# Kernel optimization log

Hardware: AMD Instinct MI355X
Metric: run time of the kernel (lower is better)

Reference implementation:

```python
import jax, jax.numpy as jnp
import numpy as np

EMBED_DIM = 512
NUM_HEADS = 8
HEAD_DIM = EMBED_DIM // NUM_HEADS
SCALE = HEAD_DIM ** -0.5
B, N = 4, 2048


def _linear_params(key, fan_in, fan_out):
    kw, kb = jax.random.split(key)
    bound = 1.0 / np.sqrt(fan_in)
    W = jax.random.uniform(kw, (fan_out, fan_in), minval=-bound, maxval=bound, dtype=jnp.float32)
    b = jax.random.uniform(kb, (fan_out,), minval=-bound, maxval=bound, dtype=jnp.float32)
    return W, b


def setup_inputs() -> dict:
    key = jax.random.key(0)
    ks = jax.random.split(key, 7)
    query = jax.random.normal(ks[0], (B, N, EMBED_DIM), dtype=jnp.float32)
    k_in = jax.random.normal(ks[1], (B, N, EMBED_DIM), dtype=jnp.float32)
    v_in = jax.random.normal(ks[2], (B, N, EMBED_DIM), dtype=jnp.float32)
    Wq, bq = _linear_params(ks[3], EMBED_DIM, EMBED_DIM)
    Wk, bk = _linear_params(ks[4], EMBED_DIM, EMBED_DIM)
    Wv, bv = _linear_params(ks[5], EMBED_DIM, EMBED_DIM)
    Wo, bo = _linear_params(ks[6], EMBED_DIM, EMBED_DIM)
    return {
        "query": query, "key": k_in, "value": v_in,
        "Wq": Wq, "bq": bq, "Wk": Wk, "bk": bk,
        "Wv": Wv, "bv": bv, "Wo": Wo, "bo": bo,
    }


def reference(query, key, value, Wq, bq, Wk, bk, Wv, bv, Wo, bo):
    Bq, Nq, _ = query.shape
    # projections: (B, S, E) x (E, E)^T + b
    q = (query @ Wq.T + bq).reshape(Bq, Nq, NUM_HEADS, HEAD_DIM).transpose(0, 2, 1, 3)  # bhnd
    k = (key @ Wk.T + bk).reshape(Bq, -1, NUM_HEADS, HEAD_DIM).transpose(0, 2, 1, 3)    # bhmd
    v = (value @ Wv.T + bv).reshape(Bq, -1, NUM_HEADS, HEAD_DIM).transpose(0, 2, 1, 3)  # bhmd
    attn = jnp.einsum('bhnd,bhmd->bhnm', q, k) * SCALE
    attn = jax.nn.softmax(attn, axis=-1)
    x = jnp.einsum('bhnm,bhmd->bhnd', attn, v)
    x = x.transpose(0, 2, 1, 3).reshape(Bq, Nq, EMBED_DIM)
    return x @ Wo.T + bo
```

## Files before the change

### kernel.cpp

```cpp
#include <hip/hip_runtime.h>
#include <stdint.h>

#define NX (8192*512)
#define NW (512*512)

typedef __bf16 bf16x8 __attribute__((ext_vector_type(8)));
typedef float  f32x4  __attribute__((ext_vector_type(4)));
typedef float  f32x16 __attribute__((ext_vector_type(16)));

__device__ __forceinline__ unsigned short f2bf(float f){
  unsigned u = __builtin_bit_cast(unsigned, f);
  u += 0x7FFFu + ((u >> 16) & 1u);
  return (unsigned short)(u >> 16);
}

__device__ __forceinline__ f32x4 mfma16(bf16x8 a, bf16x8 b, f32x4 c){
  return __builtin_amdgcn_mfma_f32_16x16x32_bf16(a, b, c, 0, 0, 0);
}
__device__ __forceinline__ f32x16 mfma32(bf16x8 a, bf16x8 b, f32x16 c){
  return __builtin_amdgcn_mfma_f32_32x32x16_bf16(a, b, c, 0, 0, 0);
}

__device__ __forceinline__ void gload_lds16(const void* g, void* l){
  __builtin_amdgcn_global_load_lds((const __attribute__((address_space(1))) void*)g,
                                   (__attribute__((address_space(3))) void*)l, 16, 0, 0);
}

#define VMCNT(n) asm volatile("s_waitcnt vmcnt(" #n ")" ::: "memory")

__global__ void convert_all(const float* __restrict__ q, const float* __restrict__ k,
                            const float* __restrict__ v, const float* __restrict__ wq,
                            const float* __restrict__ wk, const float* __restrict__ wv,
                            const float* __restrict__ wo, unsigned short* __restrict__ dst)
{
  const long total4 = (3L*NX + 4L*NW) / 4;
  for (long i = (long)blockIdx.x*blockDim.x + threadIdx.x; i < total4; i += (long)gridDim.x*blockDim.x){
    long e = i*4;
    const float* src; long off;
    if (e < NX)            { src = q;  off = e; }
    else if (e < 2L*NX)    { src = k;  off = e - NX; }
    else if (e < 3L*NX)    { src = v;  off = e - 2L*NX; }
    else {
      long w = e - 3L*NX; int wi = (int)(w / NW); off = w - (long)wi*NW;
      src = (wi==0) ? wq : (wi==1) ? wk : (wi==2) ? wv : wo;
    }
    float4 f = *(const float4*)(src + off);
    ushort4 o; o.x=f2bf(f.x); o.y=f2bf(f.y); o.z=f2bf(f.z); o.w=f2bf(f.w);
    *(ushort4*)(dst + e) = o;
  }
}

struct GArg {
  const unsigned short* A;
  const unsigned short* B;
  const float* bias;
  void* C;
  float scale;
  int mode;
};

__global__ __launch_bounds__(256) void gemm_bt(GArg g0, GArg g1, GArg g2)
{
  GArg g = (blockIdx.z==0) ? g0 : (blockIdx.z==1) ? g1 : g2;
  __shared__ __attribute__((aligned(16))) unsigned char lds[65536];
  const int tid  = threadIdx.x;
  const int lane = tid & 63;
  const int wid  = tid >> 6;
  const int wr = wid >> 1, wc = wid & 1;
  const int m0 = blockIdx.y * 128;
  const int n0 = blockIdx.x * 128;

  f32x4 acc[4][4];
  #pragma unroll
  for (int s=0;s<4;s++)
    #pragma unroll
    for (int t=0;t<4;t++) acc[s][t] = (f32x4){0.f,0.f,0.f,0.f};

  auto stage = [&](int kt, int buf){
    int Lb = tid*16;
    #pragma unroll
    for (int i=0;i<4;i++){
      int L = Lb + i*4096;
      int row = L >> 7;
      int innerS = (L & 127) ^ ((row & 7) << 4);
      gload_lds16(g.A + (size_t)(m0+row)*512 + kt*64 + (innerS>>1), lds + buf*16384 + L);
    }
    #pragma unroll
    for (int i=0;i<4;i++){
      int L = Lb + i*4096;
      int row = L >> 7;
      int innerS = (L & 127) ^ ((row & 7) << 4);
      gload_lds16(g.B + (size_t)(n0+row)*512 + kt*64 + (innerS>>1), lds + 32768 + buf*16384 + L);
    }
  };

  stage(0, 0);
  VMCNT(0);
  __syncthreads();

  for (int kt=0; kt<8; kt++){
    int cur = kt & 1;
    if (kt < 7) stage(kt+1, cur^1);
    const unsigned char* LA = lds + cur*16384;
    const unsigned char* LB = lds + 32768 + cur*16384;
    #pragma unroll
    for (int ks=0; ks<2; ks++){
      bf16x8 af[4], bfr[4];
      #pragma unroll
      for (int s=0;s<4;s++){
        int row = wr*64 + s*16 + (lane & 15);
        int inner = (ks*32 + (lane>>4)*8)*2;
        af[s] = *(const bf16x8*)(LA + row*128 + (inner ^ ((row&7)<<4)));
      }
      #pragma unroll
      for (int t=0;t<4;t++){
        int row = wc*64 + t*16 + (lane & 15);
        int inner = (ks*32 + (lane>>4)*8)*2;
        bfr[t] = *(const bf16x8*)(LB + row*128 + (inner ^ ((row&7)<<4)));
      }
      #pragma unroll
      for (int s=0;s<4;s++)
        #pragma unroll
        for (int t=0;t<4;t++)
          acc[s][t] = mfma16(af[s], bfr[t], acc[s][t]);
    }
    VMCNT(0);
    __syncthreads();
  }

  if (g.mode == 2){
    float* C = (float*)g.C;
    #pragma unroll
    for (int t=0;t<4;t++){
      int col = n0 + wc*64 + t*16 + (lane&15);
      float bv = g.bias[col];
      #pragma unroll
      for (int s=0;s<4;s++){
        #pragma unroll
        for (int r=0;r<4;r++){
          int row = m0 + wr*64 + s*16 + (lane>>4)*4 + r;
          C[(size_t)row*512 + col] = acc[s][t][r] + bv;
        }
      }
    }
  } else if (g.mode == 0){
    unsigned short* C = (unsigned short*)g.C;
    #pragma unroll
    for (int t=0;t<4;t++){
      int col = n0 + wc*64 + t*16 + (lane&15);
      float bv = g.bias[col];
      #pragma unroll
      for (int s=0;s<4;s++){
        #pragma unroll
        for (int r=0;r<4;r++){
          int row = m0 + wr*64 + s*16 + (lane>>4)*4 + r;
          C[(size_t)row*512 + col] = f2bf((acc[s][t][r] + bv) * g.scale);
        }
      }
    }
  } else {
    __syncthreads();
    unsigned short* T = (unsigned short*)lds;
    #pragma unroll
    for (int s=0;s<4;s++){
      #pragma unroll
      for (int t=0;t<4;t++){
        int col  = wc*64 + t*16 + (lane&15);
        int rowb = wr*64 + s*16 + (lane>>4)*4;
        float bv = g.bias[n0+col];
        ushort4 pk;
        pk.x = f2bf(acc[s][t][0] + bv);
        pk.y = f2bf(acc[s][t][1] + bv);
        pk.z = f2bf(acc[s][t][2] + bv);
        pk.w = f2bf(acc[s][t][3] + bv);
        *(ushort4*)(T + col*136 + rowb) = pk;
      }
    }
    __syncthreads();
    unsigned short* Vt = (unsigned short*)g.C;
    int col = tid >> 1, half = tid & 1;
    int gcol = n0 + col;
    int hh = gcol >> 6, d = gcol & 63;
    int b = m0 >> 11, ms = m0 & 2047;
    unsigned short* dst = Vt + (((size_t)(b*8+hh)*64 + d)*2048 + ms + half*64);
    const unsigned short* srcT = T + col*136 + half*64;
    #pragma unroll
    for (int j=0;j<8;j++)
      *(int4*)(dst + j*8) = *(const int4*)(srcT + j*8);
  }
}

__global__ __launch_bounds__(256) void attn_kernel(
    const unsigned short* __restrict__ Qs,
    const unsigned short* __restrict__ Kb,
    const unsigned short* __restrict__ Vt,
    unsigned short* __restrict__ AO)
{
  __shared__ __attribute__((aligned(16))) unsigned char lds[27648];
  const int tid = threadIdx.x, lane = tid & 63, wid = tid >> 6;
  const int hi = lane >> 5, lq = lane & 31;

  const int flat = blockIdx.y*16 + blockIdx.x;
  const int work = (flat & 7)*64 + (flat >> 3);
  const int bh = work >> 4, qtile = work & 15;
  const int b = bh >> 3, h = bh & 7;
  const int q0 = qtile*128 + wid*32;

  const unsigned short* Kbase = Kb + (size_t)b*2048*512 + h*64;
  const unsigned short* Vbase = Vt + (size_t)bh*64*2048;
  unsigned char* VLDS = lds + 12288;

  bf16x8 qf[4];
  #pragma unroll
  for (int c=0;c<4;c++)
    qf[c] = *(const bf16x8*)(Qs + (size_t)(b*2048 + q0 + lq)*512 + h*64 + c*16 + hi*8);

  int koff[4], voff[2][2];
  #pragma unroll
  for (int c=0;c<4;c++)
    koff[c] = lq*128 + ((c*32 + hi*16) ^ ((lq & 7) << 4));
  #pragma unroll
  for (int dh=0;dh<2;dh++)
    #pragma unroll
    for (int cb=0;cb<2;cb++)
      voff[dh][cb] = (dh*32 + lq)*80 + cb*32 + hi*16;

  const int sL = tid >> 3;
  const int sI = (tid & 7) * 16;
  const int sArow = (sL&3) + 4*((sL>>3)&1) + 8*((sL>>2)&1) + 16*((sL>>4)&1);
  const int sSrc = ((sI ^ ((sL & 7) << 4)) >> 1);
  const int vrow = wid*16 + (lane & 15);
  const int vpart = lane >> 4;

  auto stageK = [&](int t, int buf){
    gload_lds16(Kbase + (size_t)(t*32 + sArow)*512 + sSrc, lds + buf*4096 + tid*16);
  };
  auto loadV = [&](int t){
    return *(const uint4*)(Vbase + (size_t)vrow*2048 + t*32 + vpart*8);
  };
  auto writeV = [&](int buf, uint4 v){
    *(uint4*)(VLDS + buf*5120 + vrow*80 + vpart*16) = v;
  };

  f32x16 o[2];
  o[0] = (f32x16)(0.f); o[1] = (f32x16)(0.f);
  float m_run = -1e30f, l_run = 0.f;

  auto qkt = [&](const unsigned char* KL) -> f32x16 {
    f32x16 S = (f32x16)(0.f);
    #pragma unroll
    for (int c=0;c<4;c++){
      bf16x8 kf = *(const bf16x8*)(KL + koff[c]);
      S = mfma32(kf, qf[c], S);
    }
    return S;
  };

  auto finish = [&](f32x16 S, const unsigned char* VL){
    float a0 = fmaxf(fmaxf(S[0],S[1]),S[2]);
    float a1 = fmaxf(fmaxf(S[3],S[4]),S[5]);
    float a2 = fmaxf(fmaxf(S[6],S[7]),S[8]);
    float a3 = fmaxf(fmaxf(S[9],S[10]),S[11]);
    float a4 = fmaxf(fmaxf(S[12],S[13]),S[14]);
    float mt = fmaxf(fmaxf(fmaxf(a0,a1),a2), fmaxf(fmaxf(a3,a4),S[15]));
    mt = fmaxf(mt, __shfl_xor(mt, 32));

    if (!__all(mt <= m_run + 11.5415603f)){
      float mn = fmaxf(m_run, mt);
      float corr = exp2f(m_run - mn);
      l_run *= corr;
      m_run = mn;
      #pragma unroll
      for (int r=0;r<16;r++){ o[0][r] *= corr; o[1][r] *= corr; }
    }

    float p[16];
    #pragma unroll
    for (int r=0;r<16;r++) p[r] = exp2f(S[r] - m_run);

    float rs = (((p[0]+p[1])+(p[2]+p[3]))+((p[4]+p[5])+(p[6]+p[7])))
             + (((p[8]+p[9])+(p[10]+p[11]))+((p[12]+p[13])+(p[14]+p[15])));
    rs += __shfl_xor(rs, 32);
    l_run += rs;

    bf16x8 pf0, pf1;
    #pragma unroll
    for (int j=0;j<8;j++){ pf0[j] = (__bf16)p[j]; pf1[j] = (__bf16)p[8+j]; }

    #pragma unroll
    for (int dh=0;dh<2;dh++){
      bf16x8 v0 = *(const bf16x8*)(VL + voff[dh][0]);
      o[dh] = mfma32(v0, pf0, o[dh]);
      bf16x8 v1 = *(const bf16x8*)(VL + voff[dh][1]);
      o[dh] = mfma32(v1, pf1, o[dh]);
    }
  };

  stageK(0, 0); stageK(1, 1);
  uint4 VgA = loadV(0);
  VMCNT(0); writeV(0, VgA);
  __syncthreads();
  VgA = loadV(1); stageK(2, 2);
  f32x16 S_a = qkt(lds);
  VMCNT(1); writeV(1, VgA);
  __syncthreads();

  for (int t=0; t<62; t+=2){
    VgA = loadV(t+2);
    stageK(t+3, t%3);
    f32x16 S_b = qkt(lds + ((t+1)%3)*4096);
    finish(S_a, VLDS + (t%3)*5120);
    VMCNT(1); writeV((t+2)%3, VgA);
    __syncthreads();
    VgA = loadV(t+3);
    if (t < 60) stageK(t+4, (t+1)%3);
    S_a = qkt(lds + ((t+2)%3)*4096);
    finish(S_b, VLDS + ((t+1)%3)*5120);
    VMCNT(1); writeV((t+3)%3, VgA);
    __syncthreads();
  }
  {
    f32x16 S_b = qkt(lds + 0*4096);
    finish(S_a, VLDS + 2*5120);
    finish(S_b, VLDS + 0*5120);
  }

  {
    float inv = 1.0f / l_run;
    unsigned short* dst = AO + (size_t)(b*2048 + q0 + lq)*512 + h*64;
    #pragma unroll
    for (int dh=0;dh<2;dh++){
      #pragma unroll
      for (int g2=0;g2<4;g2++){
        ushort4 pk;
        pk.x = f2bf(o[dh][g2*4+0]*inv);
        pk.y = f2bf(o[dh][g2*4+1]*inv);
        pk.z = f2bf(o[dh][g2*4+2]*inv);
        pk.w = f2bf(o[dh][g2*4+3]*inv);
        *(ushort4*)(dst + dh*32 + g2*8 + hi*4) = pk;
      }
    }
  }
}

extern "C" void kernel_launch(void* const* d_in, const int* in_sizes, int n_in,
                              void* d_out, int out_size, void* d_ws, size_t ws_size,
                              hipStream_t stream)
{
  const float* q  = (const float*)d_in[0];
  const float* k  = (const float*)d_in[1];
  const float* v  = (const float*)d_in[2];
  const float* Wq = (const float*)d_in[3];
  const float* bq = (const float*)d_in[4];
  const float* Wk = (const float*)d_in[5];
  const float* bk = (const float*)d_in[6];
  const float* Wv = (const float*)d_in[7];
  const float* bv = (const float*)d_in[8];
  const float* Wo = (const float*)d_in[9];
  const float* bo = (const float*)d_in[10];

  unsigned short* X   = (unsigned short*)d_ws;
  unsigned short* Xq  = X;
  unsigned short* Xk  = X + NX;
  unsigned short* Xv  = X + 2*(size_t)NX;
  unsigned short* WqB = X + 3*(size_t)NX;
  unsigned short* WkB = WqB + NW;
  unsigned short* WvB = WqB + 2*(size_t)NW;
  unsigned short* WoB = WqB + 3*(size_t)NW;
  unsigned short* QS  = WqB + 4*(size_t)NW;
  unsigned short* KB  = QS + NX;
  unsigned short* VT  = KB + NX;
  unsigned short* AO  = VT + NX;

  convert_all<<<dim3(2048), dim3(256), 0, stream>>>(q, k, v, Wq, Wk, Wv, Wo, X);

  GArg gq{Xq, WqB, bq, (void*)QS, 0.180336878f, 0};
  GArg gk{Xk, WkB, bk, (void*)KB, 1.0f,   0};
  GArg gv{Xv, WvB, bv, (void*)VT, 1.0f,   1};
  gemm_bt<<<dim3(4, 64, 3), dim3(256), 0, stream>>>(gq, gk, gv);

  attn_kernel<<<dim3(16, 32), dim3(256), 0, stream>>>(QS, KB, VT, AO);

  GArg go{AO, WoB, bo, d_out, 1.0f, 2};
  gemm_bt<<<dim3(4, 64, 1), dim3(256), 0, stream>>>(go, go, go);
}
```

Measured before the change: 119.1 us.

## Switch attention to 16x16 MFMA tiles with 16-query waves and doubled grid

Rewrites the attention kernel to use 16x16x32 MFMA instead of 32x32x16, so each wave handles 16 queries instead of 32. The block's query tile shrinks to 64 and the grid doubles to 1024 blocks, with launch bounds asking for 4 blocks per CU. The K LDS swizzle and the softmax row reductions change to match the new layout, and per-row corrections pass through a small LDS scratch buffer. The aim is more parallelism and occupancy, but every K/V tile is now loaded by twice as many blocks, and the output is written with scalar 2-byte stores.

```diff
diff --git a/kernel.cpp b/kernel.cpp
--- a/kernel.cpp
+++ b/kernel.cpp
@@ -6,7 +6,6 @@
 
 typedef __bf16 bf16x8 __attribute__((ext_vector_type(8)));
 typedef float  f32x4  __attribute__((ext_vector_type(4)));
-typedef float  f32x16 __attribute__((ext_vector_type(16)));
 
 __device__ __forceinline__ unsigned short f2bf(float f){
   unsigned u = __builtin_bit_cast(unsigned, f);
@@ -16,9 +15,6 @@
 
 __device__ __forceinline__ f32x4 mfma16(bf16x8 a, bf16x8 b, f32x4 c){
   return __builtin_amdgcn_mfma_f32_16x16x32_bf16(a, b, c, 0, 0, 0);
-}
-__device__ __forceinline__ f32x16 mfma32(bf16x8 a, bf16x8 b, f32x16 c){
-  return __builtin_amdgcn_mfma_f32_32x32x16_bf16(a, b, c, 0, 0, 0);
 }
 
 __device__ __forceinline__ void gload_lds16(const void* g, void* l){
@@ -190,50 +186,51 @@
   }
 }
 
-__global__ __launch_bounds__(256) void attn_kernel(
+__global__ __launch_bounds__(256, 4) void attn_kernel(
     const unsigned short* __restrict__ Qs,
     const unsigned short* __restrict__ Kb,
     const unsigned short* __restrict__ Vt,
     unsigned short* __restrict__ AO)
 {
   __shared__ __attribute__((aligned(16))) unsigned char lds[27648];
+  __shared__ float scratch[4][16];
   const int tid = threadIdx.x, lane = tid & 63, wid = tid >> 6;
-  const int hi = lane >> 5, lq = lane & 31;
-
-  const int flat = blockIdx.y*16 + blockIdx.x;
-  const int work = (flat & 7)*64 + (flat >> 3);
-  const int bh = work >> 4, qtile = work & 15;
+  const int g = lane >> 4, lq = lane & 15;
+
+  const int flat = blockIdx.y*32 + blockIdx.x;
+  const int work = (flat & 7)*128 + (flat >> 3);
+  const int bh = work >> 5, qtile = work & 31;
   const int b = bh >> 3, h = bh & 7;
-  const int q0 = qtile*128 + wid*32;
+  const int q0 = qtile*64 + wid*16;
 
   const unsigned short* Kbase = Kb + (size_t)b*2048*512 + h*64;
   const unsigned short* Vbase = Vt + (size_t)bh*64*2048;
   unsigned char* VLDS = lds + 12288;
 
-  bf16x8 qf[4];
+  bf16x8 qf[2];
   #pragma unroll
-  for (int c=0;c<4;c++)
-    qf[c] = *(const bf16x8*)(Qs + (size_t)(b*2048 + q0 + lq)*512 + h*64 + c*16 + hi*8);
-
-  int koff[4], voff[2][2];
+  for (int c=0;c<2;c++)
+    qf[c] = *(const bf16x8*)(Qs + (size_t)(b*2048 + q0 + lq)*512 + h*64 + c*32 + g*8);
+
+  int koff[2][2];
   #pragma unroll
-  for (int c=0;c<4;c++)
-    koff[c] = lq*128 + ((c*32 + hi*16) ^ ((lq & 7) << 4));
-  #pragma unroll
-  for (int dh=0;dh<2;dh++)
-    #pragma unroll
-    for (int cb=0;cb<2;cb++)
-      voff[dh][cb] = (dh*32 + lq)*80 + cb*32 + hi*16;
+  for (int cb=0; cb<2; cb++){
+    int row = (lq>>2)*8 + cb*4 + (lq&3);
+    int fr = ((row & 3) << 4) | (((row >> 3) & 1) << 6);
+    #pragma unroll
+    for (int c=0;c<2;c++)
+      koff[cb][c] = row*128 + ((c*64 + g*16) ^ fr);
+  }
 
   const int sL = tid >> 3;
   const int sI = (tid & 7) * 16;
-  const int sArow = (sL&3) + 4*((sL>>3)&1) + 8*((sL>>2)&1) + 16*((sL>>4)&1);
-  const int sSrc = ((sI ^ ((sL & 7) << 4)) >> 1);
+  const int fS = ((sL & 3) << 4) | (((sL >> 3) & 1) << 6);
+  const int sSrc = ((sI ^ fS) >> 1);
   const int vrow = wid*16 + (lane & 15);
   const int vpart = lane >> 4;
 
   auto stageK = [&](int t, int buf){
-    gload_lds16(Kbase + (size_t)(t*32 + sArow)*512 + sSrc, lds + buf*4096 + tid*16);
+    gload_lds16(Kbase + (size_t)(t*32 + sL)*512 + sSrc, lds + buf*4096 + tid*16);
   };
   auto loadV = [&](int t){
     return *(const uint4*)(Vbase + (size_t)vrow*2048 + t*32 + vpart*8);
@@ -242,27 +239,30 @@
     *(uint4*)(VLDS + buf*5120 + vrow*80 + vpart*16) = v;
   };
 
-  f32x16 o[2];
-  o[0] = (f32x16)(0.f); o[1] = (f32x16)(0.f);
+  f32x4 o[4];
+  #pragma unroll
+  for (int dt=0;dt<4;dt++) o[dt] = (f32x4){0.f,0.f,0.f,0.f};
   float m_run = -1e30f, l_run = 0.f;
 
-  auto qkt = [&](const unsigned char* KL) -> f32x16 {
-    f32x16 S = (f32x16)(0.f);
-    #pragma unroll
-    for (int c=0;c<4;c++){
-      bf16x8 kf = *(const bf16x8*)(KL + koff[c]);
-      S = mfma32(kf, qf[c], S);
-    }
+  struct S2 { f32x4 s0, s1; };
+
+  auto qkt = [&](const unsigned char* KL) -> S2 {
+    bf16x8 k00 = *(const bf16x8*)(KL + koff[0][0]);
+    bf16x8 k01 = *(const bf16x8*)(KL + koff[0][1]);
+    bf16x8 k10 = *(const bf16x8*)(KL + koff[1][0]);
+    bf16x8 k11 = *(const bf16x8*)(KL + koff[1][1]);
+    S2 S;
+    S.s0 = mfma16(k00, qf[0], (f32x4){0.f,0.f,0.f,0.f});
+    S.s0 = mfma16(k01, qf[1], S.s0);
+    S.s1 = mfma16(k10, qf[0], (f32x4){0.f,0.f,0.f,0.f});
+    S.s1 = mfma16(k11, qf[1], S.s1);
     return S;
   };
 
-  auto finish = [&](f32x16 S, const unsigned char* VL){
-    float a0 = fmaxf(fmaxf(S[0],S[1]),S[2]);
-    float a1 = fmaxf(fmaxf(S[3],S[4]),S[5]);
-    float a2 = fmaxf(fmaxf(S[6],S[7]),S[8]);
-    float a3 = fmaxf(fmaxf(S[9],S[10]),S[11]);
-    float a4 = fmaxf(fmaxf(S[12],S[13]),S[14]);
-    float mt = fmaxf(fmaxf(fmaxf(a0,a1),a2), fmaxf(fmaxf(a3,a4),S[15]));
+  auto finish = [&](S2 S, const unsigned char* VL){
+    float mt = fmaxf(fmaxf(fmaxf(S.s0[0],S.s0[1]), fmaxf(S.s0[2],S.s0[3])),
+                     fmaxf(fmaxf(S.s1[0],S.s1[1]), fmaxf(S.s1[2],S.s1[3])));
+    mt = fmaxf(mt, __shfl_xor(mt, 16));
     mt = fmaxf(mt, __shfl_xor(mt, 32));
 
     if (!__all(mt <= m_run + 11.5415603f)){
@@ -270,29 +270,33 @@
       float corr = exp2f(m_run - mn);
       l_run *= corr;
       m_run = mn;
-      #pragma unroll
-      for (int r=0;r<16;r++){ o[0][r] *= corr; o[1][r] *= corr; }
-    }
-
-    float p[16];
-    #pragma unroll
-    for (int r=0;r<16;r++) p[r] = exp2f(S[r] - m_run);
-
-    float rs = (((p[0]+p[1])+(p[2]+p[3]))+((p[4]+p[5])+(p[6]+p[7])))
-             + (((p[8]+p[9])+(p[10]+p[11]))+((p[12]+p[13])+(p[14]+p[15])));
+      if (lane < 16) scratch[wid][lq] = corr;
+      f32x4 c4 = *(const f32x4*)(&scratch[wid][g*4]);
+      #pragma unroll
+      for (int dt=0;dt<4;dt++)
+        #pragma unroll
+        for (int r=0;r<4;r++) o[dt][r] *= c4[r];
+    }
+
+    float p0[4], p1[4];
+    #pragma unroll
+    for (int r=0;r<4;r++){
+      p0[r] = exp2f(S.s0[r] - m_run);
+      p1[r] = exp2f(S.s1[r] - m_run);
+    }
+    float rs = ((p0[0]+p0[1])+(p0[2]+p0[3])) + ((p1[0]+p1[1])+(p1[2]+p1[3]));
+    rs += __shfl_xor(rs, 16);
     rs += __shfl_xor(rs, 32);
     l_run += rs;
 
-    bf16x8 pf0, pf1;
-    #pragma unroll
-    for (int j=0;j<8;j++){ pf0[j] = (__bf16)p[j]; pf1[j] = (__bf16)p[8+j]; }
-
-    #pragma unroll
-    for (int dh=0;dh<2;dh++){
-      bf16x8 v0 = *(const bf16x8*)(VL + voff[dh][0]);
-      o[dh] = mfma32(v0, pf0, o[dh]);
-      bf16x8 v1 = *(const bf16x8*)(VL + voff[dh][1]);
-      o[dh] = mfma32(v1, pf1, o[dh]);
+    bf16x8 pf;
+    #pragma unroll
+    for (int r=0;r<4;r++){ pf[r] = (__bf16)p0[r]; pf[4+r] = (__bf16)p1[r]; }
+
+    #pragma unroll
+    for (int dt=0;dt<4;dt++){
+      bf16x8 vf = *(const bf16x8*)(VL + (dt*16 + lq)*80 + g*16);
+      o[dt] = mfma16(pf, vf, o[dt]);
     }
   };
 
@@ -301,14 +305,14 @@
   VMCNT(0); writeV(0, VgA);
   __syncthreads();
   VgA = loadV(1); stageK(2, 2);
-  f32x16 S_a = qkt(lds);
+  S2 S_a = qkt(lds);
   VMCNT(1); writeV(1, VgA);
   __syncthreads();
 
   for (int t=0; t<62; t+=2){
     VgA = loadV(t+2);
     stageK(t+3, t%3);
-    f32x16 S_b = qkt(lds + ((t+1)%3)*4096);
+    S2 S_b = qkt(lds + ((t+1)%3)*4096);
     finish(S_a, VLDS + (t%3)*5120);
     VMCNT(1); writeV((t+2)%3, VgA);
     __syncthreads();
@@ -320,24 +324,21 @@
     __syncthreads();
   }
   {
-    f32x16 S_b = qkt(lds + 0*4096);
+    S2 S_b = qkt(lds + 0*4096);
     finish(S_a, VLDS + 2*5120);
     finish(S_b, VLDS + 0*5120);
   }
 
   {
-    float inv = 1.0f / l_run;
-    unsigned short* dst = AO + (size_t)(b*2048 + q0 + lq)*512 + h*64;
-    #pragma unroll
-    for (int dh=0;dh<2;dh++){
-      #pragma unroll
-      for (int g2=0;g2<4;g2++){
-        ushort4 pk;
-        pk.x = f2bf(o[dh][g2*4+0]*inv);
-        pk.y = f2bf(o[dh][g2*4+1]*inv);
-        pk.z = f2bf(o[dh][g2*4+2]*inv);
-        pk.w = f2bf(o[dh][g2*4+3]*inv);
-        *(ushort4*)(dst + dh*32 + g2*8 + hi*4) = pk;
+    if (lane < 16) scratch[wid][lq] = 1.0f / l_run;
+    f32x4 li = *(const f32x4*)(&scratch[wid][g*4]);
+    #pragma unroll
+    for (int dt=0;dt<4;dt++){
+      int col = h*64 + dt*16 + lq;
+      #pragma unroll
+      for (int r=0;r<4;r++){
+        int row = b*2048 + q0 + g*4 + r;
+        AO[(size_t)row*512 + col] = f2bf(o[dt][r] * li[r]);
       }
     }
   }
@@ -379,7 +380,7 @@
   GArg gv{Xv, WvB, bv, (void*)VT, 1.0f,   1};
   gemm_bt<<<dim3(4, 64, 3), dim3(256), 0, stream>>>(gq, gk, gv);
 
-  attn_kernel<<<dim3(16, 32), dim3(256), 0, stream>>>(QS, KB, VT, AO);
+  attn_kernel<<<dim3(32, 32), dim3(256), 0, stream>>>(QS, KB, VT, AO);
 
   GArg go{AO, WoB, bo, d_out, 1.0f, 2};
   gemm_bt<<<dim3(4, 64, 1), dim3(256), 0, stream>>>(go, go, go);
```

Result: slower. 128.5 us (+7.9%).

## Split attention KV sequence across two wave groups per block and merge

Applied to the files above, without the earlier changes.

Each attention block now runs 512 threads. Two groups of four waves each process half of the key/value sequence (1024 keys) for the same 128 query rows, using separate LDS buffers. The partial outputs and running max/sum from the second group go through LDS, and the first group merges them with the usual online-softmax rescale before writing out. This halves the serial KV loop per wave and doubles the waves available to hide latency. The cost is doubled LDS use per block, an extra merge step with a sync, and possibly lower block occupancy.

```diff
diff --git a/kernel.cpp b/kernel.cpp
--- a/kernel.cpp
+++ b/kernel.cpp
@@ -190,53 +190,56 @@
   }
 }
 
-__global__ __launch_bounds__(256) void attn_kernel(
+__global__ __launch_bounds__(512, 4) void attn_kernel(
     const unsigned short* __restrict__ Qs,
     const unsigned short* __restrict__ Kb,
     const unsigned short* __restrict__ Vt,
     unsigned short* __restrict__ AO)
 {
-  __shared__ __attribute__((aligned(16))) unsigned char lds[27648];
+  __shared__ __attribute__((aligned(16))) unsigned char lds[55296];
   const int tid = threadIdx.x, lane = tid & 63, wid = tid >> 6;
+  const int half = wid >> 2, widh = wid & 3, tid_h = tid & 255;
   const int hi = lane >> 5, lq = lane & 31;
 
   const int flat = blockIdx.y*16 + blockIdx.x;
   const int work = (flat & 7)*64 + (flat >> 3);
   const int bh = work >> 4, qtile = work & 15;
   const int b = bh >> 3, h = bh & 7;
-  const int q0 = qtile*128 + wid*32;
-
-  const unsigned short* Kbase = Kb + (size_t)b*2048*512 + h*64;
-  const unsigned short* Vbase = Vt + (size_t)bh*64*2048;
-  unsigned char* VLDS = lds + 12288;
+  const int q0 = qtile*128 + widh*32;
+
+  const unsigned short* KbaseH = Kb + (size_t)b*2048*512 + h*64 + (size_t)half*1024*512;
+  const unsigned short* VbaseH = Vt + (size_t)bh*64*2048 + half*1024;
+  unsigned char* KLDS = lds + half*12288;
+  unsigned char* VLDS = lds + 24576 + half*15360;
 
   bf16x8 qf[4];
   #pragma unroll
   for (int c=0;c<4;c++)
     qf[c] = *(const bf16x8*)(Qs + (size_t)(b*2048 + q0 + lq)*512 + h*64 + c*16 + hi*8);
 
-  int koff[4], voff[2][2];
+  int koff[4];
   #pragma unroll
   for (int c=0;c<4;c++)
     koff[c] = lq*128 + ((c*32 + hi*16) ^ ((lq & 7) << 4));
+  int voff[2][2];
   #pragma unroll
   for (int dh=0;dh<2;dh++)
     #pragma unroll
     for (int cb=0;cb<2;cb++)
       voff[dh][cb] = (dh*32 + lq)*80 + cb*32 + hi*16;
 
-  const int sL = tid >> 3;
-  const int sI = (tid & 7) * 16;
+  const int sL = tid_h >> 3;
+  const int sI = (tid_h & 7) * 16;
   const int sArow = (sL&3) + 4*((sL>>3)&1) + 8*((sL>>2)&1) + 16*((sL>>4)&1);
   const int sSrc = ((sI ^ ((sL & 7) << 4)) >> 1);
-  const int vrow = wid*16 + (lane & 15);
+  const int vrow = widh*16 + (lane & 15);
   const int vpart = lane >> 4;
 
   auto stageK = [&](int t, int buf){
-    gload_lds16(Kbase + (size_t)(t*32 + sArow)*512 + sSrc, lds + buf*4096 + tid*16);
+    gload_lds16(KbaseH + (size_t)(t*32 + sArow)*512 + sSrc, KLDS + buf*4096 + tid_h*16);
   };
   auto loadV = [&](int t){
-    return *(const uint4*)(Vbase + (size_t)vrow*2048 + t*32 + vpart*8);
+    return *(const uint4*)(VbaseH + (size_t)vrow*2048 + t*32 + vpart*8);
   };
   auto writeV = [&](int buf, uint4 v){
     *(uint4*)(VLDS + buf*5120 + vrow*80 + vpart*16) = v;
@@ -246,7 +249,8 @@
   o[0] = (f32x16)(0.f); o[1] = (f32x16)(0.f);
   float m_run = -1e30f, l_run = 0.f;
 
-  auto qkt = [&](const unsigned char* KL) -> f32x16 {
+  auto qkt = [&](int buf) -> f32x16 {
+    const unsigned char* KL = KLDS + buf*4096;
     f32x16 S = (f32x16)(0.f);
     #pragma unroll
     for (int c=0;c<4;c++){
@@ -256,7 +260,8 @@
     return S;
   };
 
-  auto finish = [&](f32x16 S, const unsigned char* VL){
+  auto finish = [&](f32x16 S, int vbuf){
+    const unsigned char* VL = VLDS + vbuf*5120;
     float a0 = fmaxf(fmaxf(S[0],S[1]),S[2]);
     float a1 = fmaxf(fmaxf(S[3],S[4]),S[5]);
     float a2 = fmaxf(fmaxf(S[6],S[7]),S[8]);
@@ -301,42 +306,66 @@
   VMCNT(0); writeV(0, VgA);
   __syncthreads();
   VgA = loadV(1); stageK(2, 2);
-  f32x16 S_a = qkt(lds);
+  f32x16 S_a = qkt(0);
   VMCNT(1); writeV(1, VgA);
   __syncthreads();
 
-  for (int t=0; t<62; t+=2){
+  for (int t=0; t<30; t+=2){
     VgA = loadV(t+2);
     stageK(t+3, t%3);
-    f32x16 S_b = qkt(lds + ((t+1)%3)*4096);
-    finish(S_a, VLDS + (t%3)*5120);
+    f32x16 S_b = qkt((t+1)%3);
+    finish(S_a, t%3);
     VMCNT(1); writeV((t+2)%3, VgA);
     __syncthreads();
     VgA = loadV(t+3);
-    if (t < 60) stageK(t+4, (t+1)%3);
-    S_a = qkt(lds + ((t+2)%3)*4096);
-    finish(S_b, VLDS + ((t+1)%3)*5120);
+    if (t < 28) stageK(t+4, (t+1)%3);
+    S_a = qkt((t+2)%3);
+    finish(S_b, (t+1)%3);
     VMCNT(1); writeV((t+3)%3, VgA);
     __syncthreads();
   }
   {
-    f32x16 S_b = qkt(lds + 0*4096);
-    finish(S_a, VLDS + 2*5120);
-    finish(S_b, VLDS + 0*5120);
-  }
-
-  {
-    float inv = 1.0f / l_run;
+    f32x16 S_b = qkt(1);
+    finish(S_a, 0);
+    finish(S_b, 1);
+  }
+
+  __syncthreads();
+  float* mo = (float*)lds + widh*2048;
+  float* ml = (float*)(lds + 53248);
+  if (half == 1){
+    #pragma unroll
+    for (int dh=0; dh<2; dh++)
+      #pragma unroll
+      for (int r=0; r<16; r++){
+        int d = dh*32 + (r&3) + 8*(r>>2) + 4*hi;
+        mo[d*32 + lq] = o[dh][r];
+      }
+    if (lane < 32){
+      ml[(widh*32 + lq)*2]     = m_run;
+      ml[(widh*32 + lq)*2 + 1] = l_run;
+    }
+  }
+  __syncthreads();
+  if (half == 0){
+    float m1 = ml[(widh*32 + lq)*2];
+    float l1 = ml[(widh*32 + lq)*2 + 1];
+    float mm = fmaxf(m_run, m1);
+    float c0 = exp2f(m_run - mm);
+    float c1 = exp2f(m1 - mm);
+    float inv = 1.0f / (l_run*c0 + l1*c1);
+    float ca = c0*inv, cb = c1*inv;
     unsigned short* dst = AO + (size_t)(b*2048 + q0 + lq)*512 + h*64;
     #pragma unroll
-    for (int dh=0;dh<2;dh++){
-      #pragma unroll
-      for (int g2=0;g2<4;g2++){
+    for (int dh=0; dh<2; dh++){
+      #pragma unroll
+      for (int g2=0; g2<4; g2++){
+        int d0 = dh*32 + g2*8 + hi*4;
         ushort4 pk;
-        pk.x = f2bf(o[dh][g2*4+0]*inv);
-        pk.y = f2bf(o[dh][g2*4+1]*inv);
-        pk.z = f2bf(o[dh][g2*4+2]*inv);
-        pk.w = f2bf(o[dh][g2*4+3]*inv);
+        pk.x = f2bf(o[dh][g2*4+0]*ca + mo[(d0+0)*32+lq]*cb);
+        pk.y = f2bf(o[dh][g2*4+1]*ca + mo[(d0+1)*32+lq]*cb);
+        pk.z = f2bf(o[dh][g2*4+2]*ca + mo[(d0+2)*32+lq]*cb);
+        pk.w = f2bf(o[dh][g2*4+3]*ca + mo[(d0+3)*32+lq]*cb);
         *(ushort4*)(dst + dh*32 + g2*8 + hi*4) = pk;
       }
     }
@@ -379,7 +408,7 @@
   GArg gv{Xv, WvB, bv, (void*)VT, 1.0f,   1};
   gemm_bt<<<dim3(4, 64, 3), dim3(256), 0, stream>>>(gq, gk, gv);
 
-  attn_kernel<<<dim3(16, 32), dim3(256), 0, stream>>>(QS, KB, VT, AO);
+  attn_kernel<<<dim3(16, 32), dim3(512), 0, stream>>>(QS, KB, VT, AO);
 
   GArg go{AO, WoB, bo, d_out, 1.0f, 2};
   gemm_bt<<<dim3(4, 64, 1), dim3(256), 0, stream>>>(go, go, go);
```

Result: faster. 111.4 us (-6.4%).
